# Kernel tuning notes

Measured on AMD Instinct MI355X. Metric: run time of the kernel, lower is better.

The kernel has to match this reference:

```python
import jax, jax.numpy as jnp
import numpy as np

N = 50000          # nodes
E = 800000         # edges (avg degree 16)
D = 128            # feature dim
MSG_EPS = 1e-7     # GENConv eps added to relu(msg)
SM_EPS = 1e-16     # pyg softmax denominator eps
BN_EPS = 1e-5
LN_EPS = 1e-5


def setup_inputs() -> dict:
    key = jax.random.key(0)
    ks = jax.random.split(key, 6)
    x = jax.random.normal(ks[0], (N, D), dtype=jnp.float32)
    edge_index = jax.random.randint(ks[1], (2, E), 0, N, dtype=jnp.int32)
    t = jnp.array(1.0, dtype=jnp.float32)
    W1 = jax.random.normal(ks[2], (D, 2 * D), dtype=jnp.float32) / np.sqrt(D).astype(np.float32)
    b1 = jnp.zeros((2 * D,), jnp.float32)
    bn_gamma = jnp.ones((2 * D,), jnp.float32)
    bn_beta = jnp.zeros((2 * D,), jnp.float32)
    W2 = jax.random.normal(ks[3], (2 * D, D), dtype=jnp.float32) / np.sqrt(2 * D).astype(np.float32)
    b2 = jnp.zeros((D,), jnp.float32)
    ln_gamma = jnp.ones((D,), jnp.float32)
    ln_beta = jnp.zeros((D,), jnp.float32)
    return {"x": x, "edge_index": edge_index, "t": t, "W1": W1, "b1": b1,
            "bn_gamma": bn_gamma, "bn_beta": bn_beta, "W2": W2, "b2": b2,
            "ln_gamma": ln_gamma, "ln_beta": ln_beta}


def reference(x, edge_index, t, W1, b1, bn_gamma, bn_beta, W2, b2, ln_gamma, ln_beta):
    src, dst = edge_index[0], edge_index[1]
    # --- GENConv message: relu(x_j) + eps  -> [E, D]
    msg = jax.nn.relu(x[src]) + MSG_EPS
    # --- softmax aggregation over incoming edges per dst node, per feature
    logits = t * msg                                            # [E, D]
    seg_max = jax.ops.segment_max(logits, dst, num_segments=N)  # [N, D]
    seg_max = jnp.where(jnp.isfinite(seg_max), seg_max, 0.0)    # empty segments -> 0
    ex = jnp.exp(logits - seg_max[dst])                         # [E, D]
    denom = jax.ops.segment_sum(ex, dst, num_segments=N)        # [N, D]
    alpha = ex / (denom[dst] + SM_EPS)                          # [E, D]
    agg = jax.ops.segment_sum(alpha * msg, dst, num_segments=N) # [N, D]
    # --- GENConv update: MLP(agg + x), MLP = Lin(D,2D)->BN->ReLU->Lin(2D,D)
    h = agg + x
    h = h @ W1 + b1                                             # [N, 2D]
    mu = jnp.mean(h, axis=0)
    var = jnp.var(h, axis=0)
    h = (h - mu) * jax.lax.rsqrt(var + BN_EPS) * bn_gamma + bn_beta
    h = jax.nn.relu(h)
    h = h @ W2 + b2                                             # [N, D]
    # --- LayerNorm -> ReLU -> (dropout p=0 noop) -> residual
    mu2 = jnp.mean(h, axis=-1, keepdims=True)
    var2 = jnp.mean(jnp.square(h - mu2), axis=-1, keepdims=True)
    h = (h - mu2) * jax.lax.rsqrt(var2 + LN_EPS) * ln_gamma + ln_beta
    h = jax.nn.relu(h)
    return x + h
```

## Files before the change

### kernel.cpp

```cpp
#include <hip/hip_runtime.h>

#define D 128
#define D2 256
#define BSH 5
#define BNODES 32
#define NBMAX 2048
#define CAP 640
#define EBLK 256
#define REP 32
#define ZWORDS (2 * REP * 256)

typedef __attribute__((ext_vector_type(8))) short short8;
typedef __attribute__((ext_vector_type(4))) float f32x4;

__device__ inline unsigned short f2b(float f) {
  unsigned u = __float_as_uint(f);
  unsigned r = (u + 0x7FFFu + ((u >> 16) & 1u)) >> 16;
  return (unsigned short)r;
}
__device__ inline float lo2f(unsigned u) { return __uint_as_float(u << 16); }
__device__ inline float hi2f(unsigned u) { return __uint_as_float(u & 0xffff0000u); }

__global__ __launch_bounds__(256) void prep_kernel(
    const float* __restrict__ x, const float* __restrict__ W1,
    const float* __restrict__ W2, const float* __restrict__ tptr,
    unsigned short* __restrict__ mb,
    unsigned short* __restrict__ W1f, unsigned short* __restrict__ W2f,
    float* __restrict__ zbase, int total4) {
  int idx = blockIdx.x * 256 + threadIdx.x;
  if (idx < 32768) {
    int k = idx >> 8, n = idx & 255;
    int t = n >> 4, m16 = n & 15;
    int kk = k >> 5, quad = (k >> 3) & 3, j = k & 7;
    W1f[(((t * 4 + kk) * 64 + quad * 16 + m16) << 3) + j] = f2b(W1[idx]);
  } else if (idx < 65536) {
    int i = idx - 32768;
    int k = i >> 7, n = i & 127;
    int t = n >> 4, m16 = n & 15;
    int kk = k >> 5, quad = (k >> 3) & 3, j = k & 7;
    W2f[(((t * 8 + kk) * 64 + quad * 16 + m16) << 3) + j] = f2b(W2[i]);
  } else if (idx < 65536 + total4) {
    int i = idx - 65536;
    float scl = tptr[0] * 1.4426950408889634f;
    float4 v = reinterpret_cast<const float4*>(x)[i];
    unsigned lo = (unsigned)f2b(scl * (fmaxf(v.x, 0.f) + 1e-7f)) |
                  ((unsigned)f2b(scl * (fmaxf(v.y, 0.f) + 1e-7f)) << 16);
    unsigned hi = (unsigned)f2b(scl * (fmaxf(v.z, 0.f) + 1e-7f)) |
                  ((unsigned)f2b(scl * (fmaxf(v.w, 0.f) + 1e-7f)) << 16);
    reinterpret_cast<uint2*>(mb)[i] = make_uint2(lo, hi);
  } else if (idx < 65536 + total4 + 32) {
    reinterpret_cast<uint2*>(mb)[idx - 65536] = make_uint2(0u, 0u);
  } else if (idx < 65536 + total4 + 32 + ZWORDS) {
    zbase[idx - (65536 + total4 + 32)] = 0.f;
  }
}

__global__ __launch_bounds__(256) void hist_kernel(const int* __restrict__ ei,
                                                   int* __restrict__ hist,
                                                   int E, int nb) {
  __shared__ int cnt[NBMAX];
  int tid = threadIdx.x, blk = blockIdx.x;
  int per = (E + EBLK - 1) / EBLK;
  int c0 = blk * per;
  int nE = min(per, E - c0);
  for (int i = tid; i < nb; i += 256) cnt[i] = 0;
  __syncthreads();
  for (int j = tid; j < nE; j += 256)
    atomicAdd(&cnt[ei[E + c0 + j] >> BSH], 1);
  __syncthreads();
  for (int i = tid; i < nb; i += 256) hist[blk * nb + i] = cnt[i];
}

__global__ __launch_bounds__(256) void scan_kernel(const int* __restrict__ hist,
                                                   int* __restrict__ start,
                                                   int* __restrict__ total, int nb) {
  __shared__ int wsum[4];
  int b = blockIdx.x;
  int t = threadIdx.x;
  int l = t & 63, w = t >> 6;
  int v = hist[t * nb + b];
  int s = v;
#pragma unroll
  for (int st = 1; st < 64; st <<= 1) {
    int u = __shfl_up(s, st, 64);
    if (l >= st) s += u;
  }
  if (l == 63) wsum[w] = s;
  __syncthreads();
  int base = 0;
#pragma unroll
  for (int i = 0; i < 4; ++i)
    if (i < w) base += wsum[i];
  start[t * nb + b] = base + s - v;
  if (t == 255) total[b] = base + s;
}

__global__ __launch_bounds__(256) void scatc_kernel(const int* __restrict__ ei,
                                                    const int* __restrict__ start,
                                                    unsigned* __restrict__ pairbuf,
                                                    int E, int nb) {
  __shared__ int run[NBMAX];
  int tid = threadIdx.x, blk = blockIdx.x;
  int per = (E + EBLK - 1) / EBLK;
  int c0 = blk * per;
  int nE = min(per, E - c0);
  for (int i = tid; i < nb; i += 256) run[i] = 0;
  __syncthreads();
  const int* srow = start + blk * nb;
  for (int j = tid; j < nE; j += 256) {
    int e = c0 + j;
    int dst = ei[E + e];
    int src = ei[e];
    int b = dst >> BSH;
    int r = srow[b] + atomicAdd(&run[b], 1);
    if (r < CAP)
      pairbuf[(size_t)b * CAP + r] =
          (unsigned)src | ((unsigned)(dst & (BNODES - 1)) << 16);
  }
}

__global__ __launch_bounds__(512) void agg2_kernel(const float* __restrict__ x,
                                                   const unsigned short* __restrict__ mb,
                                                   const unsigned* __restrict__ pairbuf,
                                                   const int* __restrict__ total,
                                                   const float* __restrict__ tptr,
                                                   unsigned short* __restrict__ h0b, int N) {
  __shared__ int soff[CAP + 4 * BNODES];
  __shared__ int cnt[BNODES], off[BNODES], run[BNODES], pcnt[BNODES];
  int b = blockIdx.x;
  int tid = threadIdx.x;
  int Eb = min(total[b], CAP);
  if (tid < BNODES) { cnt[tid] = 0; run[tid] = 0; }
  __syncthreads();
  for (int j = tid; j < Eb; j += 512)
    atomicAdd(&cnt[pairbuf[(size_t)b * CAP + j] >> 16], 1);
  __syncthreads();
  if (tid < BNODES) {
    int c = cnt[tid];
    int pc = (c + 3) & ~3;
    pcnt[tid] = pc;
    int s = pc;
#pragma unroll
    for (int st = 1; st < 32; st <<= 1) {
      int u = __shfl_up(s, st, 32);
      if ((tid & 31) >= st) s += u;
    }
    off[tid] = s - pc;
  }
  __syncthreads();
  for (int j = tid; j < Eb; j += 512) {
    unsigned p = pairbuf[(size_t)b * CAP + j];
    int dl = p >> 16;
    int r = atomicAdd(&run[dl], 1);
    soff[off[dl] + r] = (int)(p & 0xffffu) << 8;
  }
  if (tid < BNODES) {
    int o = off[tid];
    for (int r = cnt[tid]; r < pcnt[tid]; ++r) soff[o + r] = N << 8;
  }
  __syncthreads();

  int w = tid >> 6;
  int l = tid & 63;
  int half = l >> 5;
  int l32 = l & 31;
  float numscale = 0.69314718055994531f / tptr[0];
  int laneoff = l32 << 3;
  const char* mbase = (const char*)mb;

#define PROC(W)                                        \
  do {                                                 \
    float u0 = lo2f((W).x), u1 = hi2f((W).x);          \
    float u2 = lo2f((W).y), u3 = hi2f((W).y);          \
    float e0, e1, e2, e3;                              \
    asm("v_exp_f32 %0, %1" : "=v"(e0) : "v"(u0));      \
    asm("v_exp_f32 %0, %1" : "=v"(e1) : "v"(u1));      \
    asm("v_exp_f32 %0, %1" : "=v"(e2) : "v"(u2));      \
    asm("v_exp_f32 %0, %1" : "=v"(e3) : "v"(u3));      \
    den0 += e0; num0 = fmaf(e0, u0, num0);             \
    den1 += e1; num1 = fmaf(e1, u1, num1);             \
    den2 += e2; num2 = fmaf(e2, u2, num2);             \
    den3 += e3; num3 = fmaf(e3, u3, num3);             \
  } while (0)

#pragma unroll
  for (int p = 0; p < 2; ++p) {
    int ln = (p << 4) | (w << 1) | half;
    int n = (b << BSH) + ln;
    if (n >= N) continue;
    int s0 = off[ln];
    int dn = pcnt[ln];
    size_t idx = ((size_t)n << 7) + (l32 << 2);
    float4 xv = *reinterpret_cast<const float4*>(x + idx);
    float den0 = 0.f, num0 = 0.f, den1 = 0.f, num1 = 0.f;
    float den2 = 0.f, num2 = 0.f, den3 = 0.f, num3 = 0.f;
    if (dn > 0) {
      uint2 uu[4];
#pragma unroll
      for (int q = 0; q < 4; ++q)
        uu[q] = *(const uint2*)(mbase + (soff[s0 + q] | laneoff));
      for (int j = 4; j < dn; j += 4) {
        uint2 vv[4];
#pragma unroll
        for (int q = 0; q < 4; ++q)
          vv[q] = *(const uint2*)(mbase + (soff[s0 + j + q] | laneoff));
#pragma unroll
        for (int q = 0; q < 4; ++q) PROC(uu[q]);
#pragma unroll
        for (int q = 0; q < 4; ++q) uu[q] = vv[q];
      }
#pragma unroll
      for (int q = 0; q < 4; ++q) PROC(uu[q]);
      float fnpad = (float)(dn - cnt[ln]);
      den0 -= fnpad; den1 -= fnpad; den2 -= fnpad; den3 -= fnpad;
    }
    float v0 = num0 * numscale / (den0 + 1e-16f) + xv.x;
    float v1 = num1 * numscale / (den1 + 1e-16f) + xv.y;
    float v2 = num2 * numscale / (den2 + 1e-16f) + xv.z;
    float v3 = num3 * numscale / (den3 + 1e-16f) + xv.w;
    uint2 o;
    o.x = (unsigned)f2b(v0) | ((unsigned)f2b(v1) << 16);
    o.y = (unsigned)f2b(v2) | ((unsigned)f2b(v3) << 16);
    *reinterpret_cast<uint2*>(h0b + idx) = o;
  }
#undef PROC
}

__global__ __launch_bounds__(256) void gemm1_stats(
    const unsigned short* __restrict__ h0b, const unsigned short* __restrict__ W1f,
    float* __restrict__ bnsum, float* __restrict__ bnsumsq, int M) {
  int tid = threadIdx.x;
  int w = tid >> 6;
  int l = tid & 63;
  int m16 = l & 15;
  int quad = l >> 4;
  int r0 = blockIdx.x * 64;

  f32x4 acc[4][4];
#pragma unroll
  for (int rt = 0; rt < 4; ++rt)
#pragma unroll
    for (int ct = 0; ct < 4; ++ct) acc[rt][ct] = (f32x4){0.f, 0.f, 0.f, 0.f};

#pragma unroll
  for (int kk = 0; kk < 4; ++kk) {
    short8 bfr[4];
#pragma unroll
    for (int ct = 0; ct < 4; ++ct)
      bfr[ct] = *reinterpret_cast<const short8*>(
          W1f + ((((w * 4 + ct) * 4 + kk) * 64 + l) << 3));
    short8 a[4];
#pragma unroll
    for (int rt = 0; rt < 4; ++rt) {
      int row = min(r0 + rt * 16 + m16, M - 1);
      a[rt] = *reinterpret_cast<const short8*>(h0b + (size_t)row * D + kk * 32 + quad * 8);
    }
#pragma unroll
    for (int rt = 0; rt < 4; ++rt)
#pragma unroll
      for (int ct = 0; ct < 4; ++ct)
        acc[rt][ct] = __builtin_amdgcn_mfma_f32_16x16x32_bf16(a[rt], bfr[ct], acc[rt][ct], 0, 0, 0);
  }

  int rep = (blockIdx.x & (REP - 1)) << 8;
#pragma unroll
  for (int ct = 0; ct < 4; ++ct) {
    int col = w * 64 + ct * 16 + m16;
    float cs = 0.f, cq = 0.f;
#pragma unroll
    for (int rt = 0; rt < 4; ++rt) {
      int rloc = rt * 16 + quad * 4;
#pragma unroll
      for (int reg = 0; reg < 4; ++reg) {
        float val = acc[rt][ct][reg];
        if (r0 + rloc + reg < M) {
          cs += val;
          cq += val * val;
        }
      }
    }
    cs += __shfl_xor(cs, 16, 64);
    cs += __shfl_xor(cs, 32, 64);
    cq += __shfl_xor(cq, 16, 64);
    cq += __shfl_xor(cq, 32, 64);
    if (quad == 0) {
      atomicAdd(&bnsum[rep + col], cs);
      atomicAdd(&bnsumsq[rep + col], cq);
    }
  }
}

__global__ __launch_bounds__(256) void gemm2_mfma(
    const unsigned short* __restrict__ h0b, const unsigned short* __restrict__ W1f,
    const unsigned short* __restrict__ W2f, const float* __restrict__ b2,
    const float* __restrict__ bnsum, const float* __restrict__ bnsumsq,
    const float* __restrict__ bng, const float* __restrict__ bnb,
    const float* __restrict__ lng, const float* __restrict__ lnb,
    const float* __restrict__ x, float* __restrict__ out, int M) {
  __shared__ unsigned short lt[4][64][72];
  __shared__ float lnp[64][2], lnp2[64][2];
  __shared__ float sS[D2], sH[D2];
  int tid = threadIdx.x;
  {
    float s = 0.f, q = 0.f;
#pragma unroll
    for (int r = 0; r < REP; ++r) {
      s += bnsum[(r << 8) + tid];
      q += bnsumsq[(r << 8) + tid];
    }
    float invM = 1.f / (float)M;
    float mu = s * invM;
    float var = q * invM - mu * mu;
    float sc = bng[tid] * rsqrtf(var + 1e-5f);
    sS[tid] = sc;
    sH[tid] = bnb[tid] - mu * sc;
  }
  __syncthreads();

  int w = tid >> 6;
  int l = tid & 63;
  int m16 = l & 15;
  int quad = l >> 4;
  int r0 = blockIdx.x * 64;

  {
    f32x4 acc[4][4];
#pragma unroll
    for (int rt = 0; rt < 4; ++rt)
#pragma unroll
      for (int ct = 0; ct < 4; ++ct) acc[rt][ct] = (f32x4){0.f, 0.f, 0.f, 0.f};

#pragma unroll
    for (int kk = 0; kk < 4; ++kk) {
      short8 bfr[4];
#pragma unroll
      for (int ct = 0; ct < 4; ++ct)
        bfr[ct] = *reinterpret_cast<const short8*>(
            W1f + ((((w * 4 + ct) * 4 + kk) * 64 + l) << 3));
      short8 a[4];
#pragma unroll
      for (int rt = 0; rt < 4; ++rt) {
        int row = min(r0 + rt * 16 + m16, M - 1);
        a[rt] = *reinterpret_cast<const short8*>(h0b + (size_t)row * D + kk * 32 + quad * 8);
      }
#pragma unroll
      for (int rt = 0; rt < 4; ++rt)
#pragma unroll
        for (int ct = 0; ct < 4; ++ct)
          acc[rt][ct] = __builtin_amdgcn_mfma_f32_16x16x32_bf16(a[rt], bfr[ct], acc[rt][ct], 0, 0, 0);
    }

#pragma unroll
    for (int ct = 0; ct < 4; ++ct) {
      int col = w * 64 + ct * 16 + m16;
      float sc = sS[col];
      float sh = sH[col];
#pragma unroll
      for (int rt = 0; rt < 4; ++rt) {
        int rloc = rt * 16 + quad * 4;
#pragma unroll
        for (int reg = 0; reg < 4; ++reg) {
          float h = fmaxf(acc[rt][ct][reg] * sc + sh, 0.f);
          lt[w][rloc + reg][ct * 16 + m16] = f2b(h);
        }
      }
    }
  }
  __syncthreads();

  int rb = w >> 1, cb = w & 1;
  f32x4 acc[2][4];
#pragma unroll
  for (int rt = 0; rt < 2; ++rt)
#pragma unroll
    for (int ct = 0; ct < 4; ++ct) acc[rt][ct] = (f32x4){0.f, 0.f, 0.f, 0.f};

#pragma unroll
  for (int kk = 0; kk < 8; ++kk) {
    int base = kk * 32 + quad * 8;
    short8 a[2];
#pragma unroll
    for (int rt = 0; rt < 2; ++rt) {
      int rl = rb * 32 + rt * 16 + m16;
      a[rt] = *reinterpret_cast<const short8*>(&lt[base >> 6][rl][base & 63]);
    }
    short8 bfr[4];
#pragma unroll
    for (int ct = 0; ct < 4; ++ct)
      bfr[ct] = *reinterpret_cast<const short8*>(
          W2f + ((((cb * 4 + ct) * 8 + kk) * 64 + l) << 3));
#pragma unroll
    for (int rt = 0; rt < 2; ++rt)
#pragma unroll
      for (int ct = 0; ct < 4; ++ct)
        acc[rt][ct] = __builtin_amdgcn_mfma_f32_16x16x32_bf16(a[rt], bfr[ct], acc[rt][ct], 0, 0, 0);
  }

  float b2v[4], lgv[4], lbv[4];
#pragma unroll
  for (int ct = 0; ct < 4; ++ct) {
    int col = cb * 64 + ct * 16 + m16;
    b2v[ct] = b2[col];
    lgv[ct] = lng[col];
    lbv[ct] = lnb[col];
  }

#pragma unroll
  for (int rt = 0; rt < 2; ++rt) {
#pragma unroll
    for (int reg = 0; reg < 4; ++reg) {
      float s = 0.f, s2 = 0.f;
#pragma unroll
      for (int ct = 0; ct < 4; ++ct) {
        float v = acc[rt][ct][reg] + b2v[ct];
        s += v;
        s2 += v * v;
      }
#pragma unroll
      for (int msk = 1; msk < 16; msk <<= 1) {
        s += __shfl_xor(s, msk, 64);
        s2 += __shfl_xor(s2, msk, 64);
      }
      if (m16 == 0) {
        int rl = rb * 32 + rt * 16 + quad * 4 + reg;
        lnp[rl][cb] = s;
        lnp2[rl][cb] = s2;
      }
    }
  }
  __syncthreads();

#pragma unroll
  for (int rt = 0; rt < 2; ++rt) {
#pragma unroll
    for (int reg = 0; reg < 4; ++reg) {
      int rl = rb * 32 + rt * 16 + quad * 4 + reg;
      int row = r0 + rl;
      float s = lnp[rl][0] + lnp[rl][1];
      float s2 = lnp2[rl][0] + lnp2[rl][1];
      float mu = s * (1.f / 128.f);
      float var = s2 * (1.f / 128.f) - mu * mu;
      float inv = rsqrtf(var + 1e-5f);
      if (row < M) {
#pragma unroll
        for (int ct = 0; ct < 4; ++ct) {
          int col = cb * 64 + ct * 16 + m16;
          float v = acc[rt][ct][reg] + b2v[ct];
          float h = fmaxf((v - mu) * inv * lgv[ct] + lbv[ct], 0.f);
          out[(size_t)row * D + col] = x[(size_t)row * D + col] + h;
        }
      }
    }
  }
}

extern "C" void kernel_launch(void* const* d_in, const int* in_sizes, int n_in,
                              void* d_out, int out_size, void* d_ws, size_t ws_size,
                              hipStream_t stream) {
  const float* x   = (const float*)d_in[0];
  const int*   ei  = (const int*)d_in[1];
  const float* t   = (const float*)d_in[2];
  const float* W1  = (const float*)d_in[3];
  const float* bng = (const float*)d_in[5];
  const float* bnb = (const float*)d_in[6];
  const float* W2  = (const float*)d_in[7];
  const float* b2  = (const float*)d_in[8];
  const float* lng = (const float*)d_in[9];
  const float* lnb = (const float*)d_in[10];
  float* out = (float*)d_out;

  int N = in_sizes[0] / D;
  int E = in_sizes[1] / 2;
  size_t nd = (size_t)N * D;
  int nb = (N + BNODES - 1) >> BSH;

  unsigned short* mb  = (unsigned short*)d_ws;
  unsigned short* h0b = mb + nd + 128;
  unsigned short* W1f = h0b + nd;
  unsigned short* W2f = W1f + 32768;
  float* bnsum   = (float*)(W2f + 32768);
  float* bnsumsq = bnsum + REP * 256;
  int* total     = (int*)(bnsumsq + REP * 256);
  int* hist      = total + NBMAX;
  int* startb    = hist + EBLK * NBMAX;
  unsigned* pairbuf = (unsigned*)(startb + EBLK * NBMAX);

  int total4 = (int)(nd / 4);
  int ptotal = 65536 + total4 + 32 + ZWORDS;
  prep_kernel<<<(ptotal + 255) / 256, 256, 0, stream>>>(x, W1, W2, t, mb, W1f, W2f,
                                                        bnsum, total4);

  hist_kernel<<<EBLK, 256, 0, stream>>>(ei, hist, E, nb);
  scan_kernel<<<nb, 256, 0, stream>>>(hist, startb, total, nb);
  scatc_kernel<<<EBLK, 256, 0, stream>>>(ei, startb, pairbuf, E, nb);
  agg2_kernel<<<nb, 512, 0, stream>>>(x, mb, pairbuf, total, t, h0b, N);

  gemm1_stats<<<(N + 63) / 64, 256, 0, stream>>>(h0b, W1f, bnsum, bnsumsq, N);
  gemm2_mfma<<<(N + 63) / 64, 256, 0, stream>>>(h0b, W1f, W2f, b2, bnsum, bnsumsq,
                                                bng, bnb, lng, lnb, x, out, N);
}
```

Measured before the change: 204.3 us.

## Fuse BN-stats GEMM into aggregation kernel and merge histogram into prep

The first-layer GEMM that gathers batch-norm column sums and sums of squares is folded into the aggregation kernel. Each block stages its 32 aggregated bf16 rows in shared memory and runs MFMA against W1 directly, so the separate gemm1 kernel no longer has to re-read h0b. The edge histogram kernel is also merged into the prep launch as extra blocks, removing one launch and letting the two overlap. The cost is a larger shared-memory footprint and an extra GEMM phase in agg2, which may lower its occupancy, plus a larger prep kernel.

```diff
diff --git a/kernel.cpp b/kernel.cpp
--- a/kernel.cpp
+++ b/kernel.cpp
@@ -8,6 +8,7 @@
 #define CAP 640
 #define EBLK 256
 #define REP 32
+#define HSTR 136
 #define ZWORDS (2 * REP * 256)
 
 typedef __attribute__((ext_vector_type(8))) short short8;
@@ -24,9 +25,25 @@
 __global__ __launch_bounds__(256) void prep_kernel(
     const float* __restrict__ x, const float* __restrict__ W1,
     const float* __restrict__ W2, const float* __restrict__ tptr,
-    unsigned short* __restrict__ mb,
+    const int* __restrict__ ei, unsigned short* __restrict__ mb,
     unsigned short* __restrict__ W1f, unsigned short* __restrict__ W2f,
-    float* __restrict__ zbase, int total4) {
+    float* __restrict__ zbase, int* __restrict__ hist,
+    int total4, int E, int nb, int pblocks) {
+  __shared__ int cnt[NBMAX];
+  if ((int)blockIdx.x >= pblocks) {
+    int blk = blockIdx.x - pblocks;
+    int tid = threadIdx.x;
+    int per = (E + EBLK - 1) / EBLK;
+    int c0 = blk * per;
+    int nE = min(per, E - c0);
+    for (int i = tid; i < nb; i += 256) cnt[i] = 0;
+    __syncthreads();
+    for (int j = tid; j < nE; j += 256)
+      atomicAdd(&cnt[ei[E + c0 + j] >> BSH], 1);
+    __syncthreads();
+    for (int i = tid; i < nb; i += 256) hist[blk * nb + i] = cnt[i];
+    return;
+  }
   int idx = blockIdx.x * 256 + threadIdx.x;
   if (idx < 32768) {
     int k = idx >> 8, n = idx & 255;
@@ -55,22 +72,6 @@
   }
 }
 
-__global__ __launch_bounds__(256) void hist_kernel(const int* __restrict__ ei,
-                                                   int* __restrict__ hist,
-                                                   int E, int nb) {
-  __shared__ int cnt[NBMAX];
-  int tid = threadIdx.x, blk = blockIdx.x;
-  int per = (E + EBLK - 1) / EBLK;
-  int c0 = blk * per;
-  int nE = min(per, E - c0);
-  for (int i = tid; i < nb; i += 256) cnt[i] = 0;
-  __syncthreads();
-  for (int j = tid; j < nE; j += 256)
-    atomicAdd(&cnt[ei[E + c0 + j] >> BSH], 1);
-  __syncthreads();
-  for (int i = tid; i < nb; i += 256) hist[blk * nb + i] = cnt[i];
-}
-
 __global__ __launch_bounds__(256) void scan_kernel(const int* __restrict__ hist,
                                                    int* __restrict__ start,
                                                    int* __restrict__ total, int nb) {
@@ -119,14 +120,15 @@
   }
 }
 
-__global__ __launch_bounds__(512) void agg2_kernel(const float* __restrict__ x,
-                                                   const unsigned short* __restrict__ mb,
-                                                   const unsigned* __restrict__ pairbuf,
-                                                   const int* __restrict__ total,
-                                                   const float* __restrict__ tptr,
-                                                   unsigned short* __restrict__ h0b, int N) {
+__global__ __launch_bounds__(512) void agg2_kernel(
+    const float* __restrict__ x, const unsigned short* __restrict__ mb,
+    const unsigned* __restrict__ pairbuf, const int* __restrict__ total,
+    const float* __restrict__ tptr, const unsigned short* __restrict__ W1f,
+    unsigned short* __restrict__ h0b, float* __restrict__ bnsum,
+    float* __restrict__ bnsumsq, int N) {
   __shared__ int soff[CAP + 4 * BNODES];
   __shared__ int cnt[BNODES], off[BNODES], run[BNODES], pcnt[BNODES];
+  __shared__ unsigned short h0t[BNODES * HSTR];
   int b = blockIdx.x;
   int tid = threadIdx.x;
   int Eb = min(total[b], CAP);
@@ -187,7 +189,11 @@
   for (int p = 0; p < 2; ++p) {
     int ln = (p << 4) | (w << 1) | half;
     int n = (b << BSH) + ln;
-    if (n >= N) continue;
+    unsigned short* lrow = &h0t[ln * HSTR + (l32 << 2)];
+    if (n >= N) {
+      *reinterpret_cast<uint2*>(lrow) = make_uint2(0u, 0u);
+      continue;
+    }
     int s0 = off[ln];
     int dn = pcnt[ln];
     size_t idx = ((size_t)n << 7) + (l32 << 2);
@@ -222,70 +228,53 @@
     o.x = (unsigned)f2b(v0) | ((unsigned)f2b(v1) << 16);
     o.y = (unsigned)f2b(v2) | ((unsigned)f2b(v3) << 16);
     *reinterpret_cast<uint2*>(h0b + idx) = o;
+    *reinterpret_cast<uint2*>(lrow) = o;
   }
 #undef PROC
-}
-
-__global__ __launch_bounds__(256) void gemm1_stats(
-    const unsigned short* __restrict__ h0b, const unsigned short* __restrict__ W1f,
-    float* __restrict__ bnsum, float* __restrict__ bnsumsq, int M) {
-  int tid = threadIdx.x;
-  int w = tid >> 6;
-  int l = tid & 63;
-  int m16 = l & 15;
-  int quad = l >> 4;
-  int r0 = blockIdx.x * 64;
-
-  f32x4 acc[4][4];
-#pragma unroll
-  for (int rt = 0; rt < 4; ++rt)
-#pragma unroll
-    for (int ct = 0; ct < 4; ++ct) acc[rt][ct] = (f32x4){0.f, 0.f, 0.f, 0.f};
-
-#pragma unroll
-  for (int kk = 0; kk < 4; ++kk) {
-    short8 bfr[4];
-#pragma unroll
-    for (int ct = 0; ct < 4; ++ct)
-      bfr[ct] = *reinterpret_cast<const short8*>(
-          W1f + ((((w * 4 + ct) * 4 + kk) * 64 + l) << 3));
-    short8 a[4];
-#pragma unroll
-    for (int rt = 0; rt < 4; ++rt) {
-      int row = min(r0 + rt * 16 + m16, M - 1);
-      a[rt] = *reinterpret_cast<const short8*>(h0b + (size_t)row * D + kk * 32 + quad * 8);
-    }
-#pragma unroll
-    for (int rt = 0; rt < 4; ++rt)
-#pragma unroll
-      for (int ct = 0; ct < 4; ++ct)
-        acc[rt][ct] = __builtin_amdgcn_mfma_f32_16x16x32_bf16(a[rt], bfr[ct], acc[rt][ct], 0, 0, 0);
-  }
-
-  int rep = (blockIdx.x & (REP - 1)) << 8;
-#pragma unroll
-  for (int ct = 0; ct < 4; ++ct) {
-    int col = w * 64 + ct * 16 + m16;
-    float cs = 0.f, cq = 0.f;
-#pragma unroll
-    for (int rt = 0; rt < 4; ++rt) {
-      int rloc = rt * 16 + quad * 4;
-#pragma unroll
-      for (int reg = 0; reg < 4; ++reg) {
-        float val = acc[rt][ct][reg];
-        if (r0 + rloc + reg < M) {
-          cs += val;
-          cq += val * val;
+  __syncthreads();
+
+  {
+    int m16 = l & 15;
+    int quad = l >> 4;
+    int t0 = w << 1;
+    f32x4 acc[2][2];
+#pragma unroll
+    for (int rt = 0; rt < 2; ++rt)
+#pragma unroll
+      for (int c = 0; c < 2; ++c) acc[rt][c] = (f32x4){0.f, 0.f, 0.f, 0.f};
+#pragma unroll
+    for (int kk = 0; kk < 4; ++kk) {
+      short8 a0 = *reinterpret_cast<const short8*>(&h0t[m16 * HSTR + kk * 32 + quad * 8]);
+      short8 a1 = *reinterpret_cast<const short8*>(&h0t[(16 + m16) * HSTR + kk * 32 + quad * 8]);
+#pragma unroll
+      for (int c = 0; c < 2; ++c) {
+        short8 bfr = *reinterpret_cast<const short8*>(
+            W1f + ((((t0 + c) * 4 + kk) * 64 + l) << 3));
+        acc[0][c] = __builtin_amdgcn_mfma_f32_16x16x32_bf16(a0, bfr, acc[0][c], 0, 0, 0);
+        acc[1][c] = __builtin_amdgcn_mfma_f32_16x16x32_bf16(a1, bfr, acc[1][c], 0, 0, 0);
+      }
+    }
+    int rep = (b & (REP - 1)) << 8;
+#pragma unroll
+    for (int c = 0; c < 2; ++c) {
+      int col = (t0 + c) * 16 + m16;
+      float cs = 0.f, cq = 0.f;
+#pragma unroll
+      for (int rt = 0; rt < 2; ++rt)
+#pragma unroll
+        for (int reg = 0; reg < 4; ++reg) {
+          float v = acc[rt][c][reg];
+          cs += v;
+          cq += v * v;
         }
-      }
-    }
-    cs += __shfl_xor(cs, 16, 64);
-    cs += __shfl_xor(cs, 32, 64);
-    cq += __shfl_xor(cq, 16, 64);
-    cq += __shfl_xor(cq, 32, 64);
-    if (quad == 0) {
-      atomicAdd(&bnsum[rep + col], cs);
-      atomicAdd(&bnsumsq[rep + col], cq);
+      cs += __shfl_xor(cs, 16, 64);
+      cs += __shfl_xor(cs, 32, 64);
+      cq += __shfl_xor(cq, 16, 64);
+      cq += __shfl_xor(cq, 32, 64);
+      if (quad == 0) {
+        atomicAdd(&bnsum[rep + col], cs);
+        atomicAdd(&bnsumsq[rep + col], cq);
+      }
     }
   }
 }
@@ -487,15 +476,15 @@
 
   int total4 = (int)(nd / 4);
   int ptotal = 65536 + total4 + 32 + ZWORDS;
-  prep_kernel<<<(ptotal + 255) / 256, 256, 0, stream>>>(x, W1, W2, t, mb, W1f, W2f,
-                                                        bnsum, total4);
-
-  hist_kernel<<<EBLK, 256, 0, stream>>>(ei, hist, E, nb);
+  int pblocks = (ptotal + 255) / 256;
+  prep_kernel<<<pblocks + EBLK, 256, 0, stream>>>(x, W1, W2, t, ei, mb, W1f, W2f,
+                                                  bnsum, hist, total4, E, nb, pblocks);
+
   scan_kernel<<<nb, 256, 0, stream>>>(hist, startb, total, nb);
   scatc_kernel<<<EBLK, 256, 0, stream>>>(ei, startb, pairbuf, E, nb);
-  agg2_kernel<<<nb, 512, 0, stream>>>(x, mb, pairbuf, total, t, h0b, N);
-
-  gemm1_stats<<<(N + 63) / 64, 256, 0, stream>>>(h0b, W1f, bnsum, bnsumsq, N);
+  agg2_kernel<<<nb, 512, 0, stream>>>(x, mb, pairbuf, total, t, W1f, h0b,
+                                      bnsum, bnsumsq, N);
+
   gemm2_mfma<<<(N + 63) / 64, 256, 0, stream>>>(h0b, W1f, W2f, b2, bnsum, bnsumsq,
                                                 bng, bnb, lng, lnb, x, out, N);
 }
```

Measured after the change: 194.7 us. 1.05x faster.
